# Optimization experiments

Measured on AMD Instinct MI355X. Metric: run time of the kernel, lower is better.

## Reference

```python
import jax, jax.numpy as jnp
import numpy as np

N_GRAPHS = 32
NUM_NODES = 2848
N = N_GRAPHS * NUM_NODES  # 91136
E = 1_000_000
K = 3   # num_stacks
T = 5   # num_layers
HID = 32
EPS = 1e-5


def setup_inputs() -> dict:
    key = jax.random.key(0)
    ks = jax.random.split(key, 32)
    s = 0.1
    rn = lambda k, shp: (jax.random.normal(k, shp, jnp.float32) * s)
    inp = {
        "x": jax.random.normal(ks[0], (N, 2), jnp.float32),
        "edge_index": jax.random.randint(ks[1], (2, E), 0, N, dtype=jnp.int32).astype(jnp.int64),
        "weights": jax.random.uniform(ks[2], (E,), jnp.float32),
        "batch": (jnp.arange(N) // NUM_NODES).astype(jnp.int64),
        # ARMAConv1: 2 -> 32
        "iw1": rn(ks[3], (K, 2, HID)),
        "w1": rn(ks[4], (T - 1, K, HID, HID)),
        "rw1": rn(ks[5], (T, K, 2, HID)),
        "b1": rn(ks[6], (T, K, 1, HID)),
        "g1": jnp.ones((HID,), jnp.float32), "be1": jnp.zeros((HID,), jnp.float32),
        # ARMAConv2: 32 -> 32
        "iw2": rn(ks[7], (K, HID, HID)),
        "w2": rn(ks[8], (T - 1, K, HID, HID)),
        "rw2": rn(ks[9], (T, K, HID, HID)),
        "b2": rn(ks[10], (T, K, 1, HID)),
        "g2": jnp.ones((HID,), jnp.float32), "be2": jnp.zeros((HID,), jnp.float32),
        # ARMAConv3: 32 -> 1
        "iw3": rn(ks[11], (K, HID, 1)),
        "w3": rn(ks[12], (T - 1, K, 1, 1)),
        "rw3": rn(ks[13], (T, K, HID, 1)),
        "b3": rn(ks[14], (T, K, 1, 1)),
        "g3": jnp.ones((1,), jnp.float32), "be3": jnp.zeros((1,), jnp.float32),
        # classifier Linear(1, 1)
        "cw": rn(ks[15], (1, 1)),
        "cb": jnp.zeros((1,), jnp.float32),
    }
    return inp


def gcn_norm(row, col, w, n):
    # deg over targets, sym normalization, no self loops (PyG ARMAConv default)
    deg = jnp.zeros((n,), w.dtype).at[col].add(w)
    dis = jnp.where(deg > 0, jax.lax.rsqrt(jnp.where(deg > 0, deg, 1.0)), 0.0)
    return dis[row] * w * dis[col]


def arma_conv(x, row, col, norm, iw, w, rw, b):
    # x: [N, Fin]; returns [N, Fout] (mean over K stacks)
    out = None
    for t in range(T):
        if t == 0:
            h = jnp.einsum('nf,kfo->kno', x, iw)          # [K, N, Fout]
        else:
            h = jnp.einsum('kno,kop->knp', out, w[t - 1])
        msg = h[:, row, :] * norm[None, :, None]           # [K, E, Fout]
        agg = jnp.zeros_like(h).at[:, col, :].add(msg)     # scatter to targets
        out = jax.nn.relu(agg + jnp.einsum('nf,kfo->kno', x, rw[t]) + b[t])
    return out.mean(axis=0)


def batch_norm(x, g, b):
    m = x.mean(axis=0)
    v = x.var(axis=0)  # biased, as torch BatchNorm1d (training stats)
    return (x - m) * jax.lax.rsqrt(v + EPS) * g + b


def reference(x, edge_index, weights, batch,
              iw1, w1, rw1, b1, g1, be1,
              iw2, w2, rw2, b2, g2, be2,
              iw3, w3, rw3, b3, g3, be3,
              cw, cb):
    row, col = edge_index[0], edge_index[1]
    norm = gcn_norm(row, col, weights, N)

    h = arma_conv(x, row, col, norm, iw1, w1, rw1, b1)
    h = jax.nn.relu(batch_norm(h, g1, be1))
    h = arma_conv(h, row, col, norm, iw2, w2, rw2, b2)
    h = jax.nn.relu(batch_norm(h, g2, be2))
    h = arma_conv(h, row, col, norm, iw3, w3, rw3, b3)
    h = jax.nn.relu(batch_norm(h, g3, be3))  # [N, 1]

    # to_dense_batch: each graph has exactly NUM_NODES nodes -> reshape
    xd = h.reshape(N_GRAPHS, NUM_NODES, 1)
    logits_nodes = (xd @ cw.T + cb).squeeze(-1)   # [B, NUM_NODES]
    logits_graph = logits_nodes.max(axis=1)       # [B]
    return logits_nodes, logits_graph
```

## Files before the change

### kernel.cpp

```cpp
#include <hip/hip_runtime.h>

#define N_GRAPHS 32
#define NUM_NODES 2848
#define NTOT (N_GRAPHS * NUM_NODES)
#define NE 1000000
#define KS 3
#define TL 5
#define HID 32
#define EPSV 1e-5f
#define SCAN_B 256
#define NBLK (NTOT / SCAN_B)
#define NBINS 64
#define CNTN (NBINS * NBLK)
#define CNTB (CNTN / SCAN_B)
#define NT8 (NTOT * 8)
#define NB16 (NTOT / 16)
#define NB32 (NTOT / 32)
#define NB64 (NTOT / 64)


__device__ __forceinline__ float2 unpk(unsigned u) {
    return make_float2(__uint_as_float(u << 16), __uint_as_float(u & 0xffff0000u));
}
__device__ __forceinline__ unsigned bf16rn(float f) {
    unsigned x = __float_as_uint(f);
    return (x + 0x7fffu + ((x >> 16) & 1u)) >> 16;
}
__device__ __forceinline__ unsigned pk(float a, float b) {
    return bf16rn(a) | (bf16rn(b) << 16);
}


__global__ void k_deg(const int* __restrict__ col, const float* __restrict__ w,
                      float* __restrict__ deg, int* __restrict__ indeg) {
    int e = blockIdx.x * blockDim.x + threadIdx.x;
    if (e < NE) {
        int c = col[e];
        atomicAdd(&deg[c], w[e]);
        atomicAdd(&indeg[c], 1);
    }
}

__global__ void k_dis(float* deg) {
    int i = blockIdx.x * blockDim.x + threadIdx.x;
    if (i < NTOT) {
        float d = deg[i];
        deg[i] = (d > 0.f) ? rsqrtf(d) : 0.f;
    }
}

__global__ void k_lhist(const int* __restrict__ indeg, int* __restrict__ cnt) {
    __shared__ int h[NBINS];
    int t = threadIdx.x;
    if (t < NBINS) h[t] = 0;
    __syncthreads();
    int n = blockIdx.x * SCAN_B + t;
    atomicAdd(&h[min(indeg[n], NBINS - 1)], 1);
    __syncthreads();
    if (t < NBINS) cnt[t * NBLK + blockIdx.x] = h[t];
}

__global__ void k_scan1(const int* __restrict__ in, int* __restrict__ bsum) {
    __shared__ int s[SCAN_B];
    int i = blockIdx.x * SCAN_B + threadIdx.x;
    s[threadIdx.x] = in[i];
    __syncthreads();
    for (int st = SCAN_B / 2; st >= 1; st >>= 1) {
        if (threadIdx.x < st) s[threadIdx.x] += s[threadIdx.x + st];
        __syncthreads();
    }
    if (threadIdx.x == 0) bsum[blockIdx.x] = s[0];
}

__global__ void k_scan2(int* __restrict__ bsum, int n) {
    __shared__ int s[512];
    int t = threadIdx.x;
    int v = (t < n) ? bsum[t] : 0;
    s[t] = v;
    __syncthreads();
    for (int off = 1; off < 512; off <<= 1) {
        int a = (t >= off) ? s[t - off] : 0;
        __syncthreads();
        s[t] += a;
        __syncthreads();
    }
    if (t < n) bsum[t] = s[t] - v;
}

__global__ void k_scan3(const int* __restrict__ in, const int* __restrict__ bsum,
                        int* __restrict__ out, int sentIdx, int sentVal) {
    __shared__ int s[SCAN_B];
    int i = blockIdx.x * SCAN_B + threadIdx.x;
    int v = in[i];
    s[threadIdx.x] = v;
    __syncthreads();
    for (int off = 1; off < SCAN_B; off <<= 1) {
        int a = (threadIdx.x >= off) ? s[threadIdx.x - off] : 0;
        __syncthreads();
        s[threadIdx.x] += a;
        __syncthreads();
    }
    out[i] = bsum[blockIdx.x] + s[threadIdx.x] - v;
    if (i == 0 && sentIdx >= 0) out[sentIdx] = sentVal;
}

__global__ void k_rank(const int* __restrict__ indeg, const int* __restrict__ cnt,
                       int* __restrict__ perm, int* __restrict__ invperm,
                       int* __restrict__ indegp) {
    __shared__ int base[NBINS];
    __shared__ int cur[NBINS];
    int t = threadIdx.x;
    if (t < NBINS) { base[t] = cnt[t * NBLK + blockIdx.x]; cur[t] = 0; }
    __syncthreads();
    int n = blockIdx.x * SCAN_B + t;
    int dg = indeg[n];
    int b = min(dg, NBINS - 1);
    int pos = base[b] + atomicAdd(&cur[b], 1);
    perm[pos] = n;
    invperm[n] = pos;
    indegp[pos] = dg;
}

__global__ void k_xp(const float2* __restrict__ x, const int* __restrict__ perm,
                     float2* __restrict__ xp) {
    int i = blockIdx.x * blockDim.x + threadIdx.x;
    if (i < NTOT) xp[i] = x[perm[i]];
}

__global__ void k_fill(const int* __restrict__ row, const int* __restrict__ col,
                       const float* __restrict__ w, const float* __restrict__ dis,
                       const int* __restrict__ invperm, int* __restrict__ cursor,
                       int2* __restrict__ adj) {
    int e = blockIdx.x * blockDim.x + threadIdx.x;
    if (e < NE) {
        int r = row[e], c = col[e];
        float nm = dis[r] * w[e] * dis[c];
        int pr = invperm[r], pc = invperm[c];
        int p = atomicAdd(&cursor[pc], 1);
        adj[p] = make_int2(pr, __float_as_int(nm));
    }
}


__global__ __launch_bounds__(256) void k_gath(
    const unsigned* __restrict__ SRC, const int* __restrict__ offs,
    const long long* __restrict__ adjq, unsigned* __restrict__ P) {
    int tid = threadIdx.x;
    int u = tid & 7;
    int nl = tid >> 3;
    int bid = blockIdx.x;
    int s = bid / NB32;
    int node = (bid - s * NB32) * 32 + nl;
    const unsigned* src = SRC + (size_t)s * NT8;
    float p0 = 0.f, p1 = 0.f;
    int e0 = offs[node], e1 = offs[node + 1];
    int e = e0;
    for (; e + 8 <= e1; e += 8) {
        long long q0 = __builtin_nontemporal_load(adjq + e);
        long long q1 = __builtin_nontemporal_load(adjq + e + 1);
        long long q2 = __builtin_nontemporal_load(adjq + e + 2);
        long long q3 = __builtin_nontemporal_load(adjq + e + 3);
        long long q4 = __builtin_nontemporal_load(adjq + e + 4);
        long long q5 = __builtin_nontemporal_load(adjq + e + 5);
        long long q6 = __builtin_nontemporal_load(adjq + e + 6);
        long long q7 = __builtin_nontemporal_load(adjq + e + 7);
        unsigned v0 = src[((unsigned)q0) * 8u + u];
        unsigned v1 = src[((unsigned)q1) * 8u + u];
        unsigned v2 = src[((unsigned)q2) * 8u + u];
        unsigned v3 = src[((unsigned)q3) * 8u + u];
        unsigned v4 = src[((unsigned)q4) * 8u + u];
        unsigned v5 = src[((unsigned)q5) * 8u + u];
        unsigned v6 = src[((unsigned)q6) * 8u + u];
        unsigned v7 = src[((unsigned)q7) * 8u + u];
        float2 t;
        float w;
        w = __int_as_float((int)(q0 >> 32)); t = unpk(v0); p0 += w * t.x; p1 += w * t.y;
        w = __int_as_float((int)(q1 >> 32)); t = unpk(v1); p0 += w * t.x; p1 += w * t.y;
        w = __int_as_float((int)(q2 >> 32)); t = unpk(v2); p0 += w * t.x; p1 += w * t.y;
        w = __int_as_float((int)(q3 >> 32)); t = unpk(v3); p0 += w * t.x; p1 += w * t.y;
        w = __int_as_float((int)(q4 >> 32)); t = unpk(v4); p0 += w * t.x; p1 += w * t.y;
        w = __int_as_float((int)(q5 >> 32)); t = unpk(v5); p0 += w * t.x; p1 += w * t.y;
        w = __int_as_float((int)(q6 >> 32)); t = unpk(v6); p0 += w * t.x; p1 += w * t.y;
        w = __int_as_float((int)(q7 >> 32)); t = unpk(v7); p0 += w * t.x; p1 += w * t.y;
    }
    for (; e + 4 <= e1; e += 4) {
        long long q0 = __builtin_nontemporal_load(adjq + e);
        long long q1 = __builtin_nontemporal_load(adjq + e + 1);
        long long q2 = __builtin_nontemporal_load(adjq + e + 2);
        long long q3 = __builtin_nontemporal_load(adjq + e + 3);
        unsigned v0 = src[((unsigned)q0) * 8u + u];
        unsigned v1 = src[((unsigned)q1) * 8u + u];
        unsigned v2 = src[((unsigned)q2) * 8u + u];
        unsigned v3 = src[((unsigned)q3) * 8u + u];
        float2 t; float w;
        w = __int_as_float((int)(q0 >> 32)); t = unpk(v0); p0 += w * t.x; p1 += w * t.y;
        w = __int_as_float((int)(q1 >> 32)); t = unpk(v1); p0 += w * t.x; p1 += w * t.y;
        w = __int_as_float((int)(q2 >> 32)); t = unpk(v2); p0 += w * t.x; p1 += w * t.y;
        w = __int_as_float((int)(q3 >> 32)); t = unpk(v3); p0 += w * t.x; p1 += w * t.y;
    }
    for (; e < e1; ++e) {
        long long q0 = __builtin_nontemporal_load(adjq + e);
        unsigned v0 = src[((unsigned)q0) * 8u + u];
        float w = __int_as_float((int)(q0 >> 32));
        float2 t = unpk(v0);
        p0 += w * t.x; p1 += w * t.y;
    }
    __builtin_nontemporal_store(pk(p0, p1), &P[(size_t)s * NT8 + (size_t)node * 8 + u]);
}


template<int FIN, bool PERK, bool LAST>
__global__ __launch_bounds__(256) void k_xform(
    const unsigned* __restrict__ P, const float* __restrict__ xin,
    const float* __restrict__ W, const float* __restrict__ rw,
    const float* __restrict__ bb, unsigned* __restrict__ OUTn,
    float* __restrict__ xm) {
    constexpr int SPK = PERK ? 3 : 1;
    constexpr int NSEC = PERK ? 6 : 2;
    constexpr int ND = 64;
    __shared__ float sp[SPK][ND][33];
    __shared__ float xr[FIN == 32 ? ND : 1][FIN == 32 ? 33 : 1];
    int tid = threadIdx.x;
    int node0 = blockIdx.x * ND;
    for (int idx = tid; idx < NSEC * ND * 8; idx += 256) {
        int s = idx / (ND * 8), r = idx % (ND * 8), n = r >> 3, u = r & 7;
        unsigned q = P[(size_t)s * NT8 + (size_t)(node0 + n) * 8 + u];
        float2 v = unpk(q);
        int kk = PERK ? (s >> 1) : 0;
        sp[kk][n][(s & 1) * 16 + u * 2] = v.x;
        sp[kk][n][(s & 1) * 16 + u * 2 + 1] = v.y;
    }
    if constexpr (FIN == 32) {
        for (int idx = tid; idx < ND * 32; idx += 256)
            xr[idx >> 5][idx & 31] = xin[(size_t)(node0 + (idx >> 5)) * 32 + (idx & 31)];
    }
    __syncthreads();
    int f2 = tid & 15, nl = tid >> 4;
    int nbase = nl * 4;
    float2 xv2[4];
    if constexpr (FIN == 2) {
#pragma unroll
        for (int n = 0; n < 4; ++n) xv2[n] = ((const float2*)xin)[node0 + nbase + n];
    }
    float m0[4] = {0.f, 0.f, 0.f, 0.f};
    float m1[4] = {0.f, 0.f, 0.f, 0.f};
#pragma unroll
    for (int k = 0; k < KS; ++k) {
        float2 bv = ((const float2*)(bb + k * HID))[f2];
        float h0[4], h1[4];
#pragma unroll
        for (int n = 0; n < 4; ++n) { h0[n] = bv.x; h1[n] = bv.y; }
        const float2* W2 = (const float2*)(W + (size_t)k * HID * HID);
        const float2* R2 = (const float2*)(rw + (size_t)k * FIN * HID);
#pragma unroll 8
        for (int i = 0; i < HID; ++i) {
            float2 wf = W2[i * 16 + f2];
            float2 rf;
            if constexpr (FIN == 32) rf = R2[i * 16 + f2];
#pragma unroll
            for (int n = 0; n < 4; ++n) {
                float s = sp[PERK ? k : 0][nbase + n][i];
                h0[n] += s * wf.x; h1[n] += s * wf.y;
                if constexpr (FIN == 32) {
                    float xv = xr[nbase + n][i];
                    h0[n] += xv * rf.x; h1[n] += xv * rf.y;
                }
            }
        }
        if constexpr (FIN == 2) {
            float2 r0 = R2[0 * 16 + f2], r1 = R2[1 * 16 + f2];
#pragma unroll
            for (int n = 0; n < 4; ++n) {
                h0[n] += xv2[n].x * r0.x + xv2[n].y * r1.x;
                h1[n] += xv2[n].x * r0.y + xv2[n].y * r1.y;
            }
        }
#pragma unroll
        for (int n = 0; n < 4; ++n) {
            h0[n] = fmaxf(h0[n], 0.f);
            h1[n] = fmaxf(h1[n], 0.f);
            if constexpr (LAST) {
                m0[n] += h0[n]; m1[n] += h1[n];
            } else {
                OUTn[(size_t)(k * 2 + (f2 >> 3)) * NT8 +
                     (size_t)(node0 + nbase + n) * 8 + (f2 & 7)] = pk(h0[n], h1[n]);
            }
        }
    }
    if constexpr (LAST) {
#pragma unroll
        for (int n = 0; n < 4; ++n) {
            xm[(size_t)(node0 + nbase + n) * 32 + 2 * f2]     = m0[n] * (1.f / 3.f);
            xm[(size_t)(node0 + nbase + n) * 32 + 2 * f2 + 1] = m1[n] * (1.f / 3.f);
        }
    }
}

__global__ __launch_bounds__(256) void k_prop0_2(
    const float2* __restrict__ xp, const float* __restrict__ iw,
    const float* __restrict__ rw0, const float* __restrict__ b0,
    const int* __restrict__ offs, const long long* __restrict__ adjq,
    unsigned* __restrict__ OUT) {
    int tid = threadIdx.x;
    int f2 = tid & 15;
    int nl = tid >> 4;
    int node = blockIdx.x * 16 + nl;
    float p0 = 0.f, p1 = 0.f;
    int e0 = offs[node], e1 = offs[node + 1];
    int e = e0;
    for (; e + 4 <= e1; e += 4) {
        long long q0 = __builtin_nontemporal_load(adjq + e);
        long long q1 = __builtin_nontemporal_load(adjq + e + 1);
        long long q2 = __builtin_nontemporal_load(adjq + e + 2);
        long long q3 = __builtin_nontemporal_load(adjq + e + 3);
        float2 x0 = xp[(unsigned)q0], x1 = xp[(unsigned)q1];
        float2 x2 = xp[(unsigned)q2], x3 = xp[(unsigned)q3];
        float w0 = __int_as_float((int)(q0 >> 32)), w1 = __int_as_float((int)(q1 >> 32));
        float w2 = __int_as_float((int)(q2 >> 32)), w3 = __int_as_float((int)(q3 >> 32));
        p0 += w0 * x0.x + w1 * x1.x + w2 * x2.x + w3 * x3.x;
        p1 += w0 * x0.y + w1 * x1.y + w2 * x2.y + w3 * x3.y;
    }
    for (; e < e1; ++e) {
        long long q0 = __builtin_nontemporal_load(adjq + e);
        float2 xs = xp[(unsigned)q0];
        float w = __int_as_float((int)(q0 >> 32));
        p0 += w * xs.x;
        p1 += w * xs.y;
    }
    float2 xn = xp[node];
#pragma unroll
    for (int k = 0; k < KS; ++k) {
        const float2* iw2 = (const float2*)(iw + k * 2 * HID);
        const float2* rw2 = (const float2*)(rw0 + k * 2 * HID);
        float2 wi0 = iw2[0 * 16 + f2], wi1 = iw2[1 * 16 + f2];
        float2 wr0 = rw2[0 * 16 + f2], wr1 = rw2[1 * 16 + f2];
        float2 bv = ((const float2*)(b0 + k * HID))[f2];
        float o0 = fmaxf(p0 * wi0.x + p1 * wi1.x + xn.x * wr0.x + xn.y * wr1.x + bv.x, 0.f);
        float o1 = fmaxf(p0 * wi0.y + p1 * wi1.y + xn.x * wr0.y + xn.y * wr1.y + bv.y, 0.f);
        OUT[(size_t)(k * 2 + (f2 >> 3)) * NT8 + (size_t)node * 8 + (f2 & 7)] = pk(o0, o1);
    }
}


__global__ void k_init1(const float* __restrict__ x, const float* __restrict__ iw,
                        float4* __restrict__ H) {
    int n = blockIdx.x * blockDim.x + threadIdx.x;
    if (n >= NTOT) return;
    float a0 = 0.f, a1 = 0.f, a2 = 0.f;
#pragma unroll
    for (int i = 0; i < HID; ++i) {
        float xv = x[n * HID + i];
        a0 += xv * iw[0 * HID + i];
        a1 += xv * iw[1 * HID + i];
        a2 += xv * iw[2 * HID + i];
    }
    H[n] = make_float4(a0, a1, a2, 0.f);
}

template<bool LAST>
__global__ void k_prop1(const float4* __restrict__ H, const float* __restrict__ xin,
                        const float* __restrict__ rw_t, const float* __restrict__ b_t,
                        const float* __restrict__ W_t, const int* __restrict__ offs,
                        const int2* __restrict__ adj, const int* __restrict__ perm,
                        float* __restrict__ outp) {
    int node = blockIdx.x * blockDim.x + threadIdx.x;
    if (node >= NTOT) return;
    float a0 = b_t[0], a1 = b_t[1], a2 = b_t[2];
#pragma unroll
    for (int i = 0; i < HID; ++i) {
        float xv = xin[node * HID + i];
        a0 += xv * rw_t[0 * HID + i];
        a1 += xv * rw_t[1 * HID + i];
        a2 += xv * rw_t[2 * HID + i];
    }
    int e0 = offs[node], e1 = offs[node + 1];
    int e = e0;
    for (; e + 4 <= e1; e += 4) {
        int2 d0 = adj[e], d1 = adj[e + 1], d2 = adj[e + 2], d3 = adj[e + 3];
        float4 h0 = H[d0.x], h1 = H[d1.x], h2 = H[d2.x], h3 = H[d3.x];
        float w0 = __int_as_float(d0.y), w1 = __int_as_float(d1.y);
        float w2 = __int_as_float(d2.y), w3 = __int_as_float(d3.y);
        a0 += w0 * h0.x; a1 += w0 * h0.y; a2 += w0 * h0.z;
        a0 += w1 * h1.x; a1 += w1 * h1.y; a2 += w1 * h1.z;
        a0 += w2 * h2.x; a1 += w2 * h2.y; a2 += w2 * h2.z;
        a0 += w3 * h3.x; a1 += w3 * h3.y; a2 += w3 * h3.z;
    }
    for (; e < e1; ++e) {
        int2 ed = adj[e];
        float4 h = H[ed.x];
        float w = __int_as_float(ed.y);
        a0 += w * h.x; a1 += w * h.y; a2 += w * h.z;
    }
    a0 = fmaxf(a0, 0.f); a1 = fmaxf(a1, 0.f); a2 = fmaxf(a2, 0.f);
    if constexpr (LAST) {
        outp[perm[node]] = (a0 + a1 + a2) * (1.f / 3.f);
    } else {
        ((float4*)outp)[node] = make_float4(a0 * W_t[0], a1 * W_t[1], a2 * W_t[2], 0.f);
    }
}


__global__ void k_bnstats(const float* __restrict__ x, float* __restrict__ stats, int F) {
    __shared__ float s1[256];
    __shared__ float s2[256];
    int tid = threadIdx.x;
    int gid = blockIdx.x * blockDim.x + tid;
    int stride = gridDim.x * blockDim.x;
    int total = NTOT * F;
    float a = 0.f, b = 0.f;
    for (int i = gid; i < total; i += stride) {
        float v = x[i];
        a += v;
        b += v * v;
    }
    s1[tid] = a; s2[tid] = b;
    __syncthreads();
    for (int s = 128; s >= F; s >>= 1) {
        if (tid < s) { s1[tid] += s1[tid + s]; s2[tid] += s2[tid + s]; }
        __syncthreads();
    }
    if (tid < F) {
        atomicAdd(&stats[tid], s1[tid]);
        atomicAdd(&stats[F + tid], s2[tid]);
    }
}

__global__ void k_bnapply32(float* __restrict__ x, const float* __restrict__ stats,
                            const float* __restrict__ g, const float* __restrict__ be,
                            unsigned* __restrict__ xbf) {
    int tid = blockIdx.x * blockDim.x + threadIdx.x;
    int f2 = tid & 15;
    int node = tid >> 4;
    int f0 = 2 * f2, f1 = f0 + 1;
    float mm0 = stats[f0] * (1.f / NTOT);
    float vv0 = stats[HID + f0] * (1.f / NTOT) - mm0 * mm0;
    float mm1 = stats[f1] * (1.f / NTOT);
    float vv1 = stats[HID + f1] * (1.f / NTOT) - mm1 * mm1;
    float y0 = fmaxf((x[(size_t)node * 32 + f0] - mm0) * rsqrtf(vv0 + EPSV) * g[f0] + be[f0], 0.f);
    float y1 = fmaxf((x[(size_t)node * 32 + f1] - mm1) * rsqrtf(vv1 + EPSV) * g[f1] + be[f1], 0.f);
    x[(size_t)node * 32 + f0] = y0;
    x[(size_t)node * 32 + f1] = y1;
    if (xbf) xbf[(size_t)(f2 >> 3) * NT8 + (size_t)node * 8 + (f2 & 7)] = pk(y0, y1);
}

__global__ void k_bnapply1(float* __restrict__ x, const float* __restrict__ stats,
                           const float* __restrict__ g, const float* __restrict__ be) {
    int i = blockIdx.x * blockDim.x + threadIdx.x;
    if (i >= NTOT) return;
    float m = stats[0] * (1.f / NTOT);
    float v = stats[1] * (1.f / NTOT) - m * m;
    float y = (x[i] - m) * rsqrtf(v + EPSV) * g[0] + be[0];
    x[i] = fmaxf(y, 0.f);
}


__global__ void k_final(const float* __restrict__ h, const float* __restrict__ cw,
                        const float* __restrict__ cb, float* __restrict__ out) {
    __shared__ float smax[256];
    int g = blockIdx.x;
    float cwv = cw[0], cbv = cb[0];
    float mx = -INFINITY;
    for (int i = threadIdx.x; i < NUM_NODES; i += blockDim.x) {
        int nidx = g * NUM_NODES + i;
        float v = h[nidx] * cwv + cbv;
        out[nidx] = v;
        mx = fmaxf(mx, v);
    }
    smax[threadIdx.x] = mx;
    __syncthreads();
    for (int s = 128; s >= 1; s >>= 1) {
        if (threadIdx.x < s) smax[threadIdx.x] = fmaxf(smax[threadIdx.x], smax[threadIdx.x + s]);
        __syncthreads();
    }
    if (threadIdx.x == 0) out[NTOT + g] = smax[0];
}


extern "C" void kernel_launch(void* const* d_in, const int* in_sizes, int n_in,
                              void* d_out, int out_size, void* d_ws, size_t ws_size,
                              hipStream_t stream) {
    const float* x   = (const float*)d_in[0];
    const int*   ei  = (const int*)d_in[1];
    const int*   row = ei;
    const int*   col = ei + NE;
    const float* wts = (const float*)d_in[2];
    const float* iw1 = (const float*)d_in[4];
    const float* w1  = (const float*)d_in[5];
    const float* rw1 = (const float*)d_in[6];
    const float* b1  = (const float*)d_in[7];
    const float* g1  = (const float*)d_in[8];
    const float* be1 = (const float*)d_in[9];
    const float* iw2 = (const float*)d_in[10];
    const float* w2  = (const float*)d_in[11];
    const float* rw2 = (const float*)d_in[12];
    const float* b2  = (const float*)d_in[13];
    const float* g2  = (const float*)d_in[14];
    const float* be2 = (const float*)d_in[15];
    const float* iw3 = (const float*)d_in[16];
    const float* w3  = (const float*)d_in[17];
    const float* rw3 = (const float*)d_in[18];
    const float* b3  = (const float*)d_in[19];
    const float* g3  = (const float*)d_in[20];
    const float* be3 = (const float*)d_in[21];
    const float* cw  = (const float*)d_in[22];
    const float* cb  = (const float*)d_in[23];
    float* out = (float*)d_out;

    char* p = (char*)d_ws;
    auto alloc = [&](size_t bytes) {
        char* r = p;
        p += (bytes + 255) & ~(size_t)255;
        return r;
    };
    float*    deg    = (float*)alloc((size_t)NTOT * 4);
    int*      indeg  = (int*)alloc((size_t)NTOT * 4);
    int*      cnt    = (int*)alloc((size_t)CNTN * 4);
    char*     zend   = p;
    int*      bsum   = (int*)alloc((size_t)NBLK * 4);
    int*      offs   = (int*)alloc((size_t)(NTOT + 1) * 4);
    int*      cursor = (int*)alloc((size_t)NTOT * 4);
    int*      perm   = (int*)alloc((size_t)NTOT * 4);
    int*      invperm= (int*)alloc((size_t)NTOT * 4);
    int*      indegp = (int*)alloc((size_t)NTOT * 4);
    int2*     adj    = (int2*)alloc((size_t)NE * 8);
    unsigned* OUTA   = (unsigned*)alloc((size_t)6 * NT8 * 4);
    unsigned* OUTB   = (unsigned*)alloc((size_t)6 * NT8 * 4);
    unsigned* P      = (unsigned*)alloc((size_t)6 * NT8 * 4);
    unsigned* xplane = (unsigned*)alloc((size_t)2 * NT8 * 4);
    float2*   xp     = (float2*)alloc((size_t)NTOT * 8);
    float*    xa     = (float*)alloc((size_t)NTOT * HID * 4);
    float*    xb     = (float*)alloc((size_t)NTOT * HID * 4);
    float*    xc     = (float*)alloc((size_t)NTOT * 4);
    float*    stats  = (float*)alloc(3 * 2 * HID * 4);
    if ((size_t)(p - (char*)d_ws) > ws_size) return;

    const int tb = 256;
    const int ebl = (NE + tb - 1) / tb;
    const int nbl = NTOT / tb;
    const long long* adjq = (const long long*)adj;

    hipMemsetAsync(deg, 0, (size_t)(zend - (char*)deg), stream);
    hipMemsetAsync(stats, 0, (size_t)3 * 2 * HID * 4, stream);

    k_deg<<<ebl, tb, 0, stream>>>(col, wts, deg, indeg);
    k_dis<<<nbl, tb, 0, stream>>>(deg);
    k_lhist<<<NBLK, SCAN_B, 0, stream>>>(indeg, cnt);
    k_scan1<<<CNTB, SCAN_B, 0, stream>>>(cnt, bsum);
    k_scan2<<<1, 512, 0, stream>>>(bsum, CNTB);
    k_scan3<<<CNTB, SCAN_B, 0, stream>>>(cnt, bsum, cnt, -1, 0);
    k_rank<<<NBLK, SCAN_B, 0, stream>>>(indeg, cnt, perm, invperm, indegp);
    k_xp<<<nbl, tb, 0, stream>>>((const float2*)x, perm, xp);
    k_scan1<<<NBLK, SCAN_B, 0, stream>>>(indegp, bsum);
    k_scan2<<<1, 512, 0, stream>>>(bsum, NBLK);
    k_scan3<<<NBLK, SCAN_B, 0, stream>>>(indegp, bsum, offs, NTOT, NE);
    hipMemcpyAsync(cursor, offs, (size_t)NTOT * 4, hipMemcpyDeviceToDevice, stream);
    k_fill<<<ebl, tb, 0, stream>>>(row, col, wts, deg, invperm, cursor, adj);

    {
        k_prop0_2<<<NB16, tb, 0, stream>>>((const float2*)xp, iw1, rw1, b1, offs, adjq, OUTA);
        unsigned* Hc = OUTA; unsigned* Hn = OUTB;
        for (int t = 1; t < TL - 1; ++t) {
            k_gath<<<6 * NB32, tb, 0, stream>>>(Hc, offs, adjq, P);
            k_xform<2, true, false><<<NB64, tb, 0, stream>>>(
                P, (const float*)xp, w1 + (size_t)(t - 1) * KS * HID * HID,
                rw1 + (size_t)t * KS * 2 * HID, b1 + (size_t)t * KS * HID, Hn, nullptr);
            unsigned* tmp = Hc; Hc = Hn; Hn = tmp;
        }
        k_gath<<<6 * NB32, tb, 0, stream>>>(Hc, offs, adjq, P);
        k_xform<2, true, true><<<NB64, tb, 0, stream>>>(
            P, (const float*)xp, w1 + (size_t)(TL - 2) * KS * HID * HID,
            rw1 + (size_t)(TL - 1) * KS * 2 * HID, b1 + (size_t)(TL - 1) * KS * HID,
            nullptr, xa);
        k_bnstats<<<256, tb, 0, stream>>>(xa, stats, HID);
        k_bnapply32<<<NTOT * 16 / tb, tb, 0, stream>>>(xa, stats, g1, be1, xplane);
    }
    {
        k_gath<<<2 * NB32, tb, 0, stream>>>(xplane, offs, adjq, P);
        k_xform<32, false, false><<<NB64, tb, 0, stream>>>(
            P, xa, iw2, rw2, b2, OUTA, nullptr);
        unsigned* Hc = OUTA; unsigned* Hn = OUTB;
        for (int t = 1; t < TL - 1; ++t) {
            k_gath<<<6 * NB32, tb, 0, stream>>>(Hc, offs, adjq, P);
            k_xform<32, true, false><<<NB64, tb, 0, stream>>>(
                P, xa, w2 + (size_t)(t - 1) * KS * HID * HID,
                rw2 + (size_t)t * KS * HID * HID, b2 + (size_t)t * KS * HID, Hn, nullptr);
            unsigned* tmp = Hc; Hc = Hn; Hn = tmp;
        }
        k_gath<<<6 * NB32, tb, 0, stream>>>(Hc, offs, adjq, P);
        k_xform<32, true, true><<<NB64, tb, 0, stream>>>(
            P, xa, w2 + (size_t)(TL - 2) * KS * HID * HID,
            rw2 + (size_t)(TL - 1) * KS * HID * HID, b2 + (size_t)(TL - 1) * KS * HID,
            nullptr, xb);
        k_bnstats<<<256, tb, 0, stream>>>(xb, stats + 2 * HID, HID);
        k_bnapply32<<<NTOT * 16 / tb, tb, 0, stream>>>(xb, stats + 2 * HID, g2, be2, nullptr);
    }
    {
        float4* HAf = (float4*)OUTA;
        float4* HBf = (float4*)OUTB;
        k_init1<<<nbl, tb, 0, stream>>>(xb, iw3, HAf);
        const float4* Hc = HAf; float4* Hn = HBf;
        for (int t = 0; t < TL - 1; ++t) {
            k_prop1<false><<<nbl, tb, 0, stream>>>(
                Hc, xb, rw3 + (size_t)t * KS * HID, b3 + (size_t)t * KS,
                w3 + (size_t)t * KS, offs, adj, perm, (float*)Hn);
            const float4* tmp = Hc; Hc = Hn; Hn = (float4*)tmp;
        }
        k_prop1<true><<<nbl, tb, 0, stream>>>(
            Hc, xb, rw3 + (size_t)(TL - 1) * KS * HID, b3 + (size_t)(TL - 1) * KS,
            nullptr, offs, adj, perm, xc);
        k_bnstats<<<256, tb, 0, stream>>>(xc, stats + 4 * HID, 1);
        k_bnapply1<<<nbl, tb, 0, stream>>>(xc, stats + 4 * HID, g3, be3);
    }

    k_final<<<N_GRAPHS, 256, 0, stream>>>(xc, cw, cb, out);
}
```

Measured before the change: 1.370 ms.

## Compress edge list to 4-byte packed index+fp16 norm and widen gather vectors

Packs each CSR edge into one 32-bit word, a 17-bit source index plus an fp16 normalization weight, which halves adjacency traffic across all propagation kernels. The gather kernel switches from 8 lanes per node with 4-byte loads to 2 lanes per node with 16-byte vector loads. The transform kernel's node tile doubles to 128 and keeps bf16 pairs packed in shared memory. Degree normalization is now computed per node from the sorted adjacency instead of with atomics, and the first layer is split into separate gather and transform kernels. The fp16 edge weights cost some precision.

```diff
diff --git a/kernel.cpp b/kernel.cpp
--- a/kernel.cpp
+++ b/kernel.cpp
@@ -1,4 +1,5 @@
 #include <hip/hip_runtime.h>
+#include <hip/hip_fp16.h>
 
 #define N_GRAPHS 32
 #define NUM_NODES 2848
@@ -14,9 +15,10 @@
 #define CNTN (NBINS * NBLK)
 #define CNTB (CNTN / SCAN_B)
 #define NT8 (NTOT * 8)
-#define NB16 (NTOT / 16)
-#define NB32 (NTOT / 32)
-#define NB64 (NTOT / 64)
+#define NB128 (NTOT / 128)
+#define SRCMASK 0x1FFFFu
+
+typedef unsigned uintx4 __attribute__((ext_vector_type(4)));
 
 
 __device__ __forceinline__ float2 unpk(unsigned u) {
@@ -29,24 +31,14 @@
 __device__ __forceinline__ unsigned pk(float a, float b) {
     return bf16rn(a) | (bf16rn(b) << 16);
 }
-
-
-__global__ void k_deg(const int* __restrict__ col, const float* __restrict__ w,
-                      float* __restrict__ deg, int* __restrict__ indeg) {
+__device__ __forceinline__ float dec_nm(unsigned q) {
+    return __half2float(__ushort_as_half((unsigned short)(q >> 17)));
+}
+
+
+__global__ void k_cnt(const int* __restrict__ col, int* __restrict__ indeg) {
     int e = blockIdx.x * blockDim.x + threadIdx.x;
-    if (e < NE) {
-        int c = col[e];
-        atomicAdd(&deg[c], w[e]);
-        atomicAdd(&indeg[c], 1);
-    }
-}
-
-__global__ void k_dis(float* deg) {
-    int i = blockIdx.x * blockDim.x + threadIdx.x;
-    if (i < NTOT) {
-        float d = deg[i];
-        deg[i] = (d > 0.f) ? rsqrtf(d) : 0.f;
-    }
+    if (e < NE) atomicAdd(&indeg[col[e]], 1);
 }
 
 __global__ void k_lhist(const int* __restrict__ indeg, int* __restrict__ cnt) {
@@ -128,84 +120,95 @@
 }
 
 __global__ void k_fill(const int* __restrict__ row, const int* __restrict__ col,
-                       const float* __restrict__ w, const float* __restrict__ dis,
-                       const int* __restrict__ invperm, int* __restrict__ cursor,
-                       int2* __restrict__ adj) {
+                       const float* __restrict__ w, const int* __restrict__ invperm,
+                       int* __restrict__ cursor, int2* __restrict__ adjtmp) {
     int e = blockIdx.x * blockDim.x + threadIdx.x;
     if (e < NE) {
-        int r = row[e], c = col[e];
-        float nm = dis[r] * w[e] * dis[c];
-        int pr = invperm[r], pc = invperm[c];
+        int pr = invperm[row[e]], pc = invperm[col[e]];
         int p = atomicAdd(&cursor[pc], 1);
-        adj[p] = make_int2(pr, __float_as_int(nm));
+        adjtmp[p] = make_int2(pr, __float_as_int(w[e]));
+    }
+}
+
+__global__ void k_degdis(const int2* __restrict__ adjtmp, const int* __restrict__ offs,
+                         float* __restrict__ disp) {
+    int n = blockIdx.x * blockDim.x + threadIdx.x;
+    if (n >= NTOT) return;
+    int e0 = offs[n], e1 = offs[n + 1];
+    float d = 0.f;
+    for (int e = e0; e < e1; ++e) d += __int_as_float(adjtmp[e].y);
+    disp[n] = (d > 0.f) ? rsqrtf(d) : 0.f;
+}
+
+__global__ void k_norm(const int2* __restrict__ adjtmp, const int* __restrict__ offs,
+                       const float* __restrict__ disp, unsigned* __restrict__ adjc) {
+    int n = blockIdx.x * blockDim.x + threadIdx.x;
+    if (n >= NTOT) return;
+    float dc = disp[n];
+    int e0 = offs[n], e1 = offs[n + 1];
+    for (int e = e0; e < e1; ++e) {
+        int2 t = adjtmp[e];
+        float nm = dc * __int_as_float(t.y) * disp[t.x];
+        unsigned short hb = __half_as_ushort(__float2half(nm));
+        adjc[e] = ((unsigned)hb << 17) | (unsigned)t.x;
     }
 }
 
 
 __global__ __launch_bounds__(256) void k_gath(
     const unsigned* __restrict__ SRC, const int* __restrict__ offs,
-    const long long* __restrict__ adjq, unsigned* __restrict__ P) {
+    const unsigned* __restrict__ adjc, unsigned* __restrict__ P) {
     int tid = threadIdx.x;
-    int u = tid & 7;
-    int nl = tid >> 3;
+    int u = tid & 1;
+    int nl = tid >> 1;
     int bid = blockIdx.x;
-    int s = bid / NB32;
-    int node = (bid - s * NB32) * 32 + nl;
-    const unsigned* src = SRC + (size_t)s * NT8;
-    float p0 = 0.f, p1 = 0.f;
+    int s = bid / NB128;
+    int node = (bid - s * NB128) * 128 + nl;
+    const uintx4* src = (const uintx4*)(SRC + (size_t)s * NT8);
+    float a0 = 0.f, a1 = 0.f, a2 = 0.f, a3 = 0.f, a4 = 0.f, a5 = 0.f, a6 = 0.f, a7 = 0.f;
     int e0 = offs[node], e1 = offs[node + 1];
     int e = e0;
-    for (; e + 8 <= e1; e += 8) {
-        long long q0 = __builtin_nontemporal_load(adjq + e);
-        long long q1 = __builtin_nontemporal_load(adjq + e + 1);
-        long long q2 = __builtin_nontemporal_load(adjq + e + 2);
-        long long q3 = __builtin_nontemporal_load(adjq + e + 3);
-        long long q4 = __builtin_nontemporal_load(adjq + e + 4);
-        long long q5 = __builtin_nontemporal_load(adjq + e + 5);
-        long long q6 = __builtin_nontemporal_load(adjq + e + 6);
-        long long q7 = __builtin_nontemporal_load(adjq + e + 7);
-        unsigned v0 = src[((unsigned)q0) * 8u + u];
-        unsigned v1 = src[((unsigned)q1) * 8u + u];
-        unsigned v2 = src[((unsigned)q2) * 8u + u];
-        unsigned v3 = src[((unsigned)q3) * 8u + u];
-        unsigned v4 = src[((unsigned)q4) * 8u + u];
-        unsigned v5 = src[((unsigned)q5) * 8u + u];
-        unsigned v6 = src[((unsigned)q6) * 8u + u];
-        unsigned v7 = src[((unsigned)q7) * 8u + u];
+    for (; e + 4 <= e1; e += 4) {
+        unsigned q0 = __builtin_nontemporal_load(adjc + e);
+        unsigned q1 = __builtin_nontemporal_load(adjc + e + 1);
+        unsigned q2 = __builtin_nontemporal_load(adjc + e + 2);
+        unsigned q3 = __builtin_nontemporal_load(adjc + e + 3);
+        uintx4 v0 = src[(q0 & SRCMASK) * 2 + u];
+        uintx4 v1 = src[(q1 & SRCMASK) * 2 + u];
+        uintx4 v2 = src[(q2 & SRCMASK) * 2 + u];
+        uintx4 v3 = src[(q3 & SRCMASK) * 2 + u];
+        float n0 = dec_nm(q0), n1 = dec_nm(q1), n2 = dec_nm(q2), n3 = dec_nm(q3);
         float2 t;
-        float w;
-        w = __int_as_float((int)(q0 >> 32)); t = unpk(v0); p0 += w * t.x; p1 += w * t.y;
-        w = __int_as_float((int)(q1 >> 32)); t = unpk(v1); p0 += w * t.x; p1 += w * t.y;
-        w = __int_as_float((int)(q2 >> 32)); t = unpk(v2); p0 += w * t.x; p1 += w * t.y;
-        w = __int_as_float((int)(q3 >> 32)); t = unpk(v3); p0 += w * t.x; p1 += w * t.y;
-        w = __int_as_float((int)(q4 >> 32)); t = unpk(v4); p0 += w * t.x; p1 += w * t.y;
-        w = __int_as_float((int)(q5 >> 32)); t = unpk(v5); p0 += w * t.x; p1 += w * t.y;
-        w = __int_as_float((int)(q6 >> 32)); t = unpk(v6); p0 += w * t.x; p1 += w * t.y;
-        w = __int_as_float((int)(q7 >> 32)); t = unpk(v7); p0 += w * t.x; p1 += w * t.y;
-    }
-    for (; e + 4 <= e1; e += 4) {
-        long long q0 = __builtin_nontemporal_load(adjq + e);
-        long long q1 = __builtin_nontemporal_load(adjq + e + 1);
-        long long q2 = __builtin_nontemporal_load(adjq + e + 2);
-        long long q3 = __builtin_nontemporal_load(adjq + e + 3);
-        unsigned v0 = src[((unsigned)q0) * 8u + u];
-        unsigned v1 = src[((unsigned)q1) * 8u + u];
-        unsigned v2 = src[((unsigned)q2) * 8u + u];
-        unsigned v3 = src[((unsigned)q3) * 8u + u];
-        float2 t; float w;
-        w = __int_as_float((int)(q0 >> 32)); t = unpk(v0); p0 += w * t.x; p1 += w * t.y;
-        w = __int_as_float((int)(q1 >> 32)); t = unpk(v1); p0 += w * t.x; p1 += w * t.y;
-        w = __int_as_float((int)(q2 >> 32)); t = unpk(v2); p0 += w * t.x; p1 += w * t.y;
-        w = __int_as_float((int)(q3 >> 32)); t = unpk(v3); p0 += w * t.x; p1 += w * t.y;
+        t = unpk(v0.x); a0 += n0 * t.x; a1 += n0 * t.y;
+        t = unpk(v0.y); a2 += n0 * t.x; a3 += n0 * t.y;
+        t = unpk(v0.z); a4 += n0 * t.x; a5 += n0 * t.y;
+        t = unpk(v0.w); a6 += n0 * t.x; a7 += n0 * t.y;
+        t = unpk(v1.x); a0 += n1 * t.x; a1 += n1 * t.y;
+        t = unpk(v1.y); a2 += n1 * t.x; a3 += n1 * t.y;
+        t = unpk(v1.z); a4 += n1 * t.x; a5 += n1 * t.y;
+        t = unpk(v1.w); a6 += n1 * t.x; a7 += n1 * t.y;
+        t = unpk(v2.x); a0 += n2 * t.x; a1 += n2 * t.y;
+        t = unpk(v2.y); a2 += n2 * t.x; a3 += n2 * t.y;
+        t = unpk(v2.z); a4 += n2 * t.x; a5 += n2 * t.y;
+        t = unpk(v2.w); a6 += n2 * t.x; a7 += n2 * t.y;
+        t = unpk(v3.x); a0 += n3 * t.x; a1 += n3 * t.y;
+        t = unpk(v3.y); a2 += n3 * t.x; a3 += n3 * t.y;
+        t = unpk(v3.z); a4 += n3 * t.x; a5 += n3 * t.y;
+        t = unpk(v3.w); a6 += n3 * t.x; a7 += n3 * t.y;
     }
     for (; e < e1; ++e) {
-        long long q0 = __builtin_nontemporal_load(adjq + e);
-        unsigned v0 = src[((unsigned)q0) * 8u + u];
-        float w = __int_as_float((int)(q0 >> 32));
-        float2 t = unpk(v0);
-        p0 += w * t.x; p1 += w * t.y;
-    }
-    __builtin_nontemporal_store(pk(p0, p1), &P[(size_t)s * NT8 + (size_t)node * 8 + u]);
+        unsigned q0 = __builtin_nontemporal_load(adjc + e);
+        uintx4 v0 = src[(q0 & SRCMASK) * 2 + u];
+        float n0 = dec_nm(q0);
+        float2 t;
+        t = unpk(v0.x); a0 += n0 * t.x; a1 += n0 * t.y;
+        t = unpk(v0.y); a2 += n0 * t.x; a3 += n0 * t.y;
+        t = unpk(v0.z); a4 += n0 * t.x; a5 += n0 * t.y;
+        t = unpk(v0.w); a6 += n0 * t.x; a7 += n0 * t.y;
+    }
+    uintx4 o;
+    o.x = pk(a0, a1); o.y = pk(a2, a3); o.z = pk(a4, a5); o.w = pk(a6, a7);
+    __builtin_nontemporal_store(o, (uintx4*)(P + (size_t)s * NT8 + (size_t)node * 8) + u);
 }
 
 
@@ -217,66 +220,78 @@
     float* __restrict__ xm) {
     constexpr int SPK = PERK ? 3 : 1;
     constexpr int NSEC = PERK ? 6 : 2;
-    constexpr int ND = 64;
-    __shared__ float sp[SPK][ND][33];
+    constexpr int ND = 128;
+    __shared__ unsigned sp[SPK][ND][17];
     __shared__ float xr[FIN == 32 ? ND : 1][FIN == 32 ? 33 : 1];
     int tid = threadIdx.x;
     int node0 = blockIdx.x * ND;
-    for (int idx = tid; idx < NSEC * ND * 8; idx += 256) {
-        int s = idx / (ND * 8), r = idx % (ND * 8), n = r >> 3, u = r & 7;
-        unsigned q = P[(size_t)s * NT8 + (size_t)(node0 + n) * 8 + u];
-        float2 v = unpk(q);
+    for (int t4 = tid; t4 < NSEC * 256; t4 += 256) {
+        int s = t4 >> 8, r = t4 & 255, n = r >> 1, u4 = (r & 1) * 4;
+        uintx4 v = *(const uintx4*)(P + (size_t)s * NT8 + (size_t)(node0 + n) * 8 + u4);
         int kk = PERK ? (s >> 1) : 0;
-        sp[kk][n][(s & 1) * 16 + u * 2] = v.x;
-        sp[kk][n][(s & 1) * 16 + u * 2 + 1] = v.y;
+        int base = (s & 1) * 8 + u4;
+        sp[kk][n][base]     = v.x;
+        sp[kk][n][base + 1] = v.y;
+        sp[kk][n][base + 2] = v.z;
+        sp[kk][n][base + 3] = v.w;
     }
     if constexpr (FIN == 32) {
-        for (int idx = tid; idx < ND * 32; idx += 256)
-            xr[idx >> 5][idx & 31] = xin[(size_t)(node0 + (idx >> 5)) * 32 + (idx & 31)];
+        for (int t4 = tid; t4 < ND * 8; t4 += 256) {
+            int n = t4 >> 3, j4 = (t4 & 7) * 4;
+            float4 v = ((const float4*)xin)[(size_t)(node0 + n) * 8 + (t4 & 7)];
+            xr[n][j4] = v.x; xr[n][j4 + 1] = v.y; xr[n][j4 + 2] = v.z; xr[n][j4 + 3] = v.w;
+        }
     }
     __syncthreads();
     int f2 = tid & 15, nl = tid >> 4;
-    int nbase = nl * 4;
-    float2 xv2[4];
+    int nbase = nl * 8;
+    float2 xv2[8];
     if constexpr (FIN == 2) {
 #pragma unroll
-        for (int n = 0; n < 4; ++n) xv2[n] = ((const float2*)xin)[node0 + nbase + n];
-    }
-    float m0[4] = {0.f, 0.f, 0.f, 0.f};
-    float m1[4] = {0.f, 0.f, 0.f, 0.f};
+        for (int n = 0; n < 8; ++n) xv2[n] = ((const float2*)xin)[node0 + nbase + n];
+    }
+    float m0[8] = {}, m1[8] = {};
 #pragma unroll
     for (int k = 0; k < KS; ++k) {
+        constexpr int kkI = 0;
+        const int kk = PERK ? k : kkI;
         float2 bv = ((const float2*)(bb + k * HID))[f2];
-        float h0[4], h1[4];
-#pragma unroll
-        for (int n = 0; n < 4; ++n) { h0[n] = bv.x; h1[n] = bv.y; }
+        float h0[8], h1[8];
+#pragma unroll
+        for (int n = 0; n < 8; ++n) { h0[n] = bv.x; h1[n] = bv.y; }
         const float2* W2 = (const float2*)(W + (size_t)k * HID * HID);
         const float2* R2 = (const float2*)(rw + (size_t)k * FIN * HID);
-#pragma unroll 8
-        for (int i = 0; i < HID; ++i) {
-            float2 wf = W2[i * 16 + f2];
-            float2 rf;
-            if constexpr (FIN == 32) rf = R2[i * 16 + f2];
-#pragma unroll
-            for (int n = 0; n < 4; ++n) {
-                float s = sp[PERK ? k : 0][nbase + n][i];
-                h0[n] += s * wf.x; h1[n] += s * wf.y;
+#pragma unroll 4
+        for (int i2 = 0; i2 < 16; ++i2) {
+            float2 wf0 = W2[(2 * i2) * 16 + f2];
+            float2 wf1 = W2[(2 * i2 + 1) * 16 + f2];
+            float2 rf0, rf1;
+            if constexpr (FIN == 32) {
+                rf0 = R2[(2 * i2) * 16 + f2];
+                rf1 = R2[(2 * i2 + 1) * 16 + f2];
+            }
+#pragma unroll
+            for (int n = 0; n < 8; ++n) {
+                float2 sv = unpk(sp[kk][nbase + n][i2]);
+                h0[n] += sv.x * wf0.x + sv.y * wf1.x;
+                h1[n] += sv.x * wf0.y + sv.y * wf1.y;
                 if constexpr (FIN == 32) {
-                    float xv = xr[nbase + n][i];
-                    h0[n] += xv * rf.x; h1[n] += xv * rf.y;
+                    float x0 = xr[nbase + n][2 * i2], x1 = xr[nbase + n][2 * i2 + 1];
+                    h0[n] += x0 * rf0.x + x1 * rf1.x;
+                    h1[n] += x0 * rf0.y + x1 * rf1.y;
                 }
             }
         }
         if constexpr (FIN == 2) {
             float2 r0 = R2[0 * 16 + f2], r1 = R2[1 * 16 + f2];
 #pragma unroll
-            for (int n = 0; n < 4; ++n) {
+            for (int n = 0; n < 8; ++n) {
                 h0[n] += xv2[n].x * r0.x + xv2[n].y * r1.x;
                 h1[n] += xv2[n].x * r0.y + xv2[n].y * r1.y;
             }
         }
 #pragma unroll
-        for (int n = 0; n < 4; ++n) {
+        for (int n = 0; n < 8; ++n) {
             h0[n] = fmaxf(h0[n], 0.f);
             h1[n] = fmaxf(h1[n], 0.f);
             if constexpr (LAST) {
@@ -289,44 +304,47 @@
     }
     if constexpr (LAST) {
 #pragma unroll
-        for (int n = 0; n < 4; ++n) {
-            xm[(size_t)(node0 + nbase + n) * 32 + 2 * f2]     = m0[n] * (1.f / 3.f);
-            xm[(size_t)(node0 + nbase + n) * 32 + 2 * f2 + 1] = m1[n] * (1.f / 3.f);
-        }
-    }
-}
-
-__global__ __launch_bounds__(256) void k_prop0_2(
-    const float2* __restrict__ xp, const float* __restrict__ iw,
-    const float* __restrict__ rw0, const float* __restrict__ b0,
-    const int* __restrict__ offs, const long long* __restrict__ adjq,
-    unsigned* __restrict__ OUT) {
-    int tid = threadIdx.x;
-    int f2 = tid & 15;
-    int nl = tid >> 4;
-    int node = blockIdx.x * 16 + nl;
-    float p0 = 0.f, p1 = 0.f;
+        for (int n = 0; n < 8; ++n)
+            ((float2*)xm)[(size_t)(node0 + nbase + n) * 16 + f2] =
+                make_float2(m0[n] * (1.f / 3.f), m1[n] * (1.f / 3.f));
+    }
+}
+
+
+__global__ void k_gath2(const float2* __restrict__ xp, const int* __restrict__ offs,
+                        const unsigned* __restrict__ adjc, float2* __restrict__ pag) {
+    int node = blockIdx.x * blockDim.x + threadIdx.x;
+    if (node >= NTOT) return;
+    float a0 = 0.f, a1 = 0.f;
     int e0 = offs[node], e1 = offs[node + 1];
     int e = e0;
     for (; e + 4 <= e1; e += 4) {
-        long long q0 = __builtin_nontemporal_load(adjq + e);
-        long long q1 = __builtin_nontemporal_load(adjq + e + 1);
-        long long q2 = __builtin_nontemporal_load(adjq + e + 2);
-        long long q3 = __builtin_nontemporal_load(adjq + e + 3);
-        float2 x0 = xp[(unsigned)q0], x1 = xp[(unsigned)q1];
-        float2 x2 = xp[(unsigned)q2], x3 = xp[(unsigned)q3];
-        float w0 = __int_as_float((int)(q0 >> 32)), w1 = __int_as_float((int)(q1 >> 32));
-        float w2 = __int_as_float((int)(q2 >> 32)), w3 = __int_as_float((int)(q3 >> 32));
-        p0 += w0 * x0.x + w1 * x1.x + w2 * x2.x + w3 * x3.x;
-        p1 += w0 * x0.y + w1 * x1.y + w2 * x2.y + w3 * x3.y;
+        unsigned q0 = __builtin_nontemporal_load(adjc + e);
+        unsigned q1 = __builtin_nontemporal_load(adjc + e + 1);
+        unsigned q2 = __builtin_nontemporal_load(adjc + e + 2);
+        unsigned q3 = __builtin_nontemporal_load(adjc + e + 3);
+        float2 x0 = xp[q0 & SRCMASK], x1 = xp[q1 & SRCMASK];
+        float2 x2 = xp[q2 & SRCMASK], x3 = xp[q3 & SRCMASK];
+        float n0 = dec_nm(q0), n1 = dec_nm(q1), n2 = dec_nm(q2), n3 = dec_nm(q3);
+        a0 += n0 * x0.x + n1 * x1.x + n2 * x2.x + n3 * x3.x;
+        a1 += n0 * x0.y + n1 * x1.y + n2 * x2.y + n3 * x3.y;
     }
     for (; e < e1; ++e) {
-        long long q0 = __builtin_nontemporal_load(adjq + e);
-        float2 xs = xp[(unsigned)q0];
-        float w = __int_as_float((int)(q0 >> 32));
-        p0 += w * xs.x;
-        p1 += w * xs.y;
-    }
+        unsigned q0 = __builtin_nontemporal_load(adjc + e);
+        float2 xs = xp[q0 & SRCMASK];
+        float nm = dec_nm(q0);
+        a0 += nm * xs.x; a1 += nm * xs.y;
+    }
+    pag[node] = make_float2(a0, a1);
+}
+
+__global__ void k_x0(const float2* __restrict__ pag, const float2* __restrict__ xp,
+                     const float* __restrict__ iw, const float* __restrict__ rw0,
+                     const float* __restrict__ b0, unsigned* __restrict__ OUT) {
+    int tid = blockIdx.x * blockDim.x + threadIdx.x;
+    int f2 = tid & 15;
+    int node = tid >> 4;
+    float2 pv = pag[node];
     float2 xn = xp[node];
 #pragma unroll
     for (int k = 0; k < KS; ++k) {
@@ -335,8 +353,8 @@
         float2 wi0 = iw2[0 * 16 + f2], wi1 = iw2[1 * 16 + f2];
         float2 wr0 = rw2[0 * 16 + f2], wr1 = rw2[1 * 16 + f2];
         float2 bv = ((const float2*)(b0 + k * HID))[f2];
-        float o0 = fmaxf(p0 * wi0.x + p1 * wi1.x + xn.x * wr0.x + xn.y * wr1.x + bv.x, 0.f);
-        float o1 = fmaxf(p0 * wi0.y + p1 * wi1.y + xn.x * wr0.y + xn.y * wr1.y + bv.y, 0.f);
+        float o0 = fmaxf(pv.x * wi0.x + pv.y * wi1.x + xn.x * wr0.x + xn.y * wr1.x + bv.x, 0.f);
+        float o1 = fmaxf(pv.x * wi0.y + pv.y * wi1.y + xn.x * wr0.y + xn.y * wr1.y + bv.y, 0.f);
         OUT[(size_t)(k * 2 + (f2 >> 3)) * NT8 + (size_t)node * 8 + (f2 & 7)] = pk(o0, o1);
     }
 }
@@ -361,7 +379,7 @@
 __global__ void k_prop1(const float4* __restrict__ H, const float* __restrict__ xin,
                         const float* __restrict__ rw_t, const float* __restrict__ b_t,
                         const float* __restrict__ W_t, const int* __restrict__ offs,
-                        const int2* __restrict__ adj, const int* __restrict__ perm,
+                        const unsigned* __restrict__ adjc, const int* __restrict__ perm,
                         float* __restrict__ outp) {
     int node = blockIdx.x * blockDim.x + threadIdx.x;
     if (node >= NTOT) return;
@@ -376,20 +394,23 @@
     int e0 = offs[node], e1 = offs[node + 1];
     int e = e0;
     for (; e + 4 <= e1; e += 4) {
-        int2 d0 = adj[e], d1 = adj[e + 1], d2 = adj[e + 2], d3 = adj[e + 3];
-        float4 h0 = H[d0.x], h1 = H[d1.x], h2 = H[d2.x], h3 = H[d3.x];
-        float w0 = __int_as_float(d0.y), w1 = __int_as_float(d1.y);
-        float w2 = __int_as_float(d2.y), w3 = __int_as_float(d3.y);
-        a0 += w0 * h0.x; a1 += w0 * h0.y; a2 += w0 * h0.z;
-        a0 += w1 * h1.x; a1 += w1 * h1.y; a2 += w1 * h1.z;
-        a0 += w2 * h2.x; a1 += w2 * h2.y; a2 += w2 * h2.z;
-        a0 += w3 * h3.x; a1 += w3 * h3.y; a2 += w3 * h3.z;
+        unsigned q0 = __builtin_nontemporal_load(adjc + e);
+        unsigned q1 = __builtin_nontemporal_load(adjc + e + 1);
+        unsigned q2 = __builtin_nontemporal_load(adjc + e + 2);
+        unsigned q3 = __builtin_nontemporal_load(adjc + e + 3);
+        float4 h0 = H[q0 & SRCMASK], h1 = H[q1 & SRCMASK];
+        float4 h2 = H[q2 & SRCMASK], h3 = H[q3 & SRCMASK];
+        float n0 = dec_nm(q0), n1 = dec_nm(q1), n2 = dec_nm(q2), n3 = dec_nm(q3);
+        a0 += n0 * h0.x; a1 += n0 * h0.y; a2 += n0 * h0.z;
+        a0 += n1 * h1.x; a1 += n1 * h1.y; a2 += n1 * h1.z;
+        a0 += n2 * h2.x; a1 += n2 * h2.y; a2 += n2 * h2.z;
+        a0 += n3 * h3.x; a1 += n3 * h3.y; a2 += n3 * h3.z;
     }
     for (; e < e1; ++e) {
-        int2 ed = adj[e];
-        float4 h = H[ed.x];
-        float w = __int_as_float(ed.y);
-        a0 += w * h.x; a1 += w * h.y; a2 += w * h.z;
+        unsigned q0 = __builtin_nontemporal_load(adjc + e);
+        float4 h = H[q0 & SRCMASK];
+        float nm = dec_nm(q0);
+        a0 += nm * h.x; a1 += nm * h.y; a2 += nm * h.z;
     }
     a0 = fmaxf(a0, 0.f); a1 = fmaxf(a1, 0.f); a2 = fmaxf(a2, 0.f);
     if constexpr (LAST) {
@@ -512,7 +533,6 @@
         p += (bytes + 255) & ~(size_t)255;
         return r;
     };
-    float*    deg    = (float*)alloc((size_t)NTOT * 4);
     int*      indeg  = (int*)alloc((size_t)NTOT * 4);
     int*      cnt    = (int*)alloc((size_t)CNTN * 4);
     char*     zend   = p;
@@ -522,12 +542,15 @@
     int*      perm   = (int*)alloc((size_t)NTOT * 4);
     int*      invperm= (int*)alloc((size_t)NTOT * 4);
     int*      indegp = (int*)alloc((size_t)NTOT * 4);
-    int2*     adj    = (int2*)alloc((size_t)NE * 8);
+    float*    disp   = (float*)alloc((size_t)NTOT * 4);
+    int2*     adjtmp = (int2*)alloc((size_t)NE * 8);
+    unsigned* adjc   = (unsigned*)alloc((size_t)NE * 4);
     unsigned* OUTA   = (unsigned*)alloc((size_t)6 * NT8 * 4);
     unsigned* OUTB   = (unsigned*)alloc((size_t)6 * NT8 * 4);
     unsigned* P      = (unsigned*)alloc((size_t)6 * NT8 * 4);
     unsigned* xplane = (unsigned*)alloc((size_t)2 * NT8 * 4);
     float2*   xp     = (float2*)alloc((size_t)NTOT * 8);
+    float2*   pag    = (float2*)alloc((size_t)NTOT * 8);
     float*    xa     = (float*)alloc((size_t)NTOT * HID * 4);
     float*    xb     = (float*)alloc((size_t)NTOT * HID * 4);
     float*    xc     = (float*)alloc((size_t)NTOT * 4);
@@ -537,13 +560,12 @@
     const int tb = 256;
     const int ebl = (NE + tb - 1) / tb;
     const int nbl = NTOT / tb;
-    const long long* adjq = (const long long*)adj;
-
-    hipMemsetAsync(deg, 0, (size_t)(zend - (char*)deg), stream);
+    const int g16 = NTOT * 16 / tb;
+
+    hipMemsetAsync(indeg, 0, (size_t)(zend - (char*)indeg), stream);
     hipMemsetAsync(stats, 0, (size_t)3 * 2 * HID * 4, stream);
 
-    k_deg<<<ebl, tb, 0, stream>>>(col, wts, deg, indeg);
-    k_dis<<<nbl, tb, 0, stream>>>(deg);
+    k_cnt<<<ebl, tb, 0, stream>>>(col, indeg);
     k_lhist<<<NBLK, SCAN_B, 0, stream>>>(indeg, cnt);
     k_scan1<<<CNTB, SCAN_B, 0, stream>>>(cnt, bsum);
     k_scan2<<<1, 512, 0, stream>>>(bsum, CNTB);
@@ -554,45 +576,48 @@
     k_scan2<<<1, 512, 0, stream>>>(bsum, NBLK);
     k_scan3<<<NBLK, SCAN_B, 0, stream>>>(indegp, bsum, offs, NTOT, NE);
     hipMemcpyAsync(cursor, offs, (size_t)NTOT * 4, hipMemcpyDeviceToDevice, stream);
-    k_fill<<<ebl, tb, 0, stream>>>(row, col, wts, deg, invperm, cursor, adj);
+    k_fill<<<ebl, tb, 0, stream>>>(row, col, wts, invperm, cursor, adjtmp);
+    k_degdis<<<nbl, tb, 0, stream>>>(adjtmp, offs, disp);
+    k_norm<<<nbl, tb, 0, stream>>>(adjtmp, offs, disp, adjc);
 
     {
-        k_prop0_2<<<NB16, tb, 0, stream>>>((const float2*)xp, iw1, rw1, b1, offs, adjq, OUTA);
+        k_gath2<<<nbl, tb, 0, stream>>>(xp, offs, adjc, pag);
+        k_x0<<<g16, tb, 0, stream>>>(pag, xp, iw1, rw1, b1, OUTA);
         unsigned* Hc = OUTA; unsigned* Hn = OUTB;
         for (int t = 1; t < TL - 1; ++t) {
-            k_gath<<<6 * NB32, tb, 0, stream>>>(Hc, offs, adjq, P);
-            k_xform<2, true, false><<<NB64, tb, 0, stream>>>(
+            k_gath<<<6 * NB128, tb, 0, stream>>>(Hc, offs, adjc, P);
+            k_xform<2, true, false><<<NB128, tb, 0, stream>>>(
                 P, (const float*)xp, w1 + (size_t)(t - 1) * KS * HID * HID,
                 rw1 + (size_t)t * KS * 2 * HID, b1 + (size_t)t * KS * HID, Hn, nullptr);
             unsigned* tmp = Hc; Hc = Hn; Hn = tmp;
         }
-        k_gath<<<6 * NB32, tb, 0, stream>>>(Hc, offs, adjq, P);
-        k_xform<2, true, true><<<NB64, tb, 0, stream>>>(
+        k_gath<<<6 * NB128, tb, 0, stream>>>(Hc, offs, adjc, P);
+        k_xform<2, true, true><<<NB128, tb, 0, stream>>>(
             P, (const float*)xp, w1 + (size_t)(TL - 2) * KS * HID * HID,
             rw1 + (size_t)(TL - 1) * KS * 2 * HID, b1 + (size_t)(TL - 1) * KS * HID,
             nullptr, xa);
         k_bnstats<<<256, tb, 0, stream>>>(xa, stats, HID);
-        k_bnapply32<<<NTOT * 16 / tb, tb, 0, stream>>>(xa, stats, g1, be1, xplane);
+        k_bnapply32<<<g16, tb, 0, stream>>>(xa, stats, g1, be1, xplane);
     }
     {
-        k_gath<<<2 * NB32, tb, 0, stream>>>(xplane, offs, adjq, P);
-        k_xform<32, false, false><<<NB64, tb, 0, stream>>>(
+        k_gath<<<2 * NB128, tb, 0, stream>>>(xplane, offs, adjc, P);
+        k_xform<32, false, false><<<NB128, tb, 0, stream>>>(
             P, xa, iw2, rw2, b2, OUTA, nullptr);
         unsigned* Hc = OUTA; unsigned* Hn = OUTB;
         for (int t = 1; t < TL - 1; ++t) {
-            k_gath<<<6 * NB32, tb, 0, stream>>>(Hc, offs, adjq, P);
-            k_xform<32, true, false><<<NB64, tb, 0, stream>>>(
+            k_gath<<<6 * NB128, tb, 0, stream>>>(Hc, offs, adjc, P);
+            k_xform<32, true, false><<<NB128, tb, 0, stream>>>(
                 P, xa, w2 + (size_t)(t - 1) * KS * HID * HID,
                 rw2 + (size_t)t * KS * HID * HID, b2 + (size_t)t * KS * HID, Hn, nullptr);
             unsigned* tmp = Hc; Hc = Hn; Hn = tmp;
         }
-        k_gath<<<6 * NB32, tb, 0, stream>>>(Hc, offs, adjq, P);
-        k_xform<32, true, true><<<NB64, tb, 0, stream>>>(
+        k_gath<<<6 * NB128, tb, 0, stream>>>(Hc, offs, adjc, P);
+        k_xform<32, true, true><<<NB128, tb, 0, stream>>>(
             P, xa, w2 + (size_t)(TL - 2) * KS * HID * HID,
             rw2 + (size_t)(TL - 1) * KS * HID * HID, b2 + (size_t)(TL - 1) * KS * HID,
             nullptr, xb);
         k_bnstats<<<256, tb, 0, stream>>>(xb, stats + 2 * HID, HID);
-        k_bnapply32<<<NTOT * 16 / tb, tb, 0, stream>>>(xb, stats + 2 * HID, g2, be2, nullptr);
+        k_bnapply32<<<g16, tb, 0, stream>>>(xb, stats + 2 * HID, g2, be2, nullptr);
     }
     {
         float4* HAf = (float4*)OUTA;
@@ -602,12 +627,12 @@
         for (int t = 0; t < TL - 1; ++t) {
             k_prop1<false><<<nbl, tb, 0, stream>>>(
                 Hc, xb, rw3 + (size_t)t * KS * HID, b3 + (size_t)t * KS,
-                w3 + (size_t)t * KS, offs, adj, perm, (float*)Hn);
+                w3 + (size_t)t * KS, offs, adjc, perm, (float*)Hn);
             const float4* tmp = Hc; Hc = Hn; Hn = (float4*)tmp;
         }
         k_prop1<true><<<nbl, tb, 0, stream>>>(
             Hc, xb, rw3 + (size_t)(TL - 1) * KS * HID, b3 + (size_t)(TL - 1) * KS,
-            nullptr, offs, adj, perm, xc);
+            nullptr, offs, adjc, perm, xc);
         k_bnstats<<<256, tb, 0, stream>>>(xc, stats + 4 * HID, 1);
         k_bnapply1<<<nbl, tb, 0, stream>>>(xc, stats + 4 * HID, g3, be3);
     }
```

Result: faster. 1.171 ms (-14.5%).
